# Kernel tuning notes

Measured on AMD Instinct MI355X. Metric: run time of the kernel, lower is better.

The kernel has to match this reference:

```python
import jax, jax.numpy as jnp
import numpy as np

B_SZ, L, D = 8, 8192, 256


def setup_inputs() -> dict:
    key = jax.random.key(0)
    kx, ka, kb, kc = jax.random.split(key, 4)
    x = jax.random.normal(kx, (B_SZ, L, D), dtype=jnp.float32)
    # Scale A so its spectral radius is < 1; otherwise the 8192-step linear
    # recurrence overflows. (Random Gaussian DxD with std s has norm ~ 2*s*sqrt(D).)
    A = jax.random.normal(ka, (D, D), dtype=jnp.float32) * (0.4 / np.sqrt(D))
    B = jax.random.normal(kb, (D, D), dtype=jnp.float32) * 0.05
    C = jax.random.normal(kc, (D, D), dtype=jnp.float32) * 0.05
    return {"x": x, "A": A, "B": B, "C": C}


def reference(x, A, B, C):
    # state_t = state_{t-1} @ A + x_t @ B.T ; out_t = state_t @ C.T
    # Dropout is identity in eval mode and omitted.
    b = x.shape[0]
    h = A.shape[0]
    init = jnp.zeros((b, h), dtype=x.dtype)
    Bt = B.T  # (input_dim, hidden_dim) -> math uses x @ B.T per source
    Ct = C.T

    def step(state, xt):  # xt: (b, d)
        state = state @ A + xt @ Bt
        return state, state @ Ct

    _, ys = jax.lax.scan(step, init, jnp.swapaxes(x, 0, 1))  # ys: (l, b, out)
    return jnp.swapaxes(ys, 0, 1)  # (b, l, out)
```

## Files before the change

### kernel.cpp

```cpp
#include <hip/hip_runtime.h>

#define BSZ 8
#define LSEQ 8192
#define DDIM 256
#define CHUNK 16
#define WARM 32
#define STEPS (CHUNK + WARM)
#define CPB 16

typedef float f32x4 __attribute__((ext_vector_type(4)));
typedef _Float16 h8 __attribute__((ext_vector_type(8)));
typedef _Float16 h4 __attribute__((ext_vector_type(4)));
typedef _Float16 h2 __attribute__((ext_vector_type(2)));


__global__ void k_cvt_mats(const float* __restrict__ A, const float* __restrict__ B,
                           const float* __restrict__ C, _Float16* __restrict__ AhT,
                           _Float16* __restrict__ Bh, _Float16* __restrict__ Ch,
                           float* __restrict__ Zp) {
  int r = blockIdx.x, c = threadIdx.x;
  AhT[c * 256 + r] = (_Float16)A[r * 256 + c];
  Bh[r * 256 + c] = (_Float16)B[r * 256 + c];
  Ch[r * 256 + c] = (_Float16)C[r * 256 + c];
  if (r == 0) Zp[c] = 0.f;
}

__global__ __launch_bounds__(256, 2) void k_gemm_u(const float* __restrict__ x,
                                                   const _Float16* __restrict__ Bh,
                                                   _Float16* __restrict__ U) {
  __shared__ __align__(16) _Float16 xh[128][264];
  const int tid = threadIdx.x, wv = tid >> 6, lane = tid & 63;
  const int l15 = lane & 15, q = lane >> 4;
  const size_t rowbase = (size_t)blockIdx.x * 128;
#pragma unroll
  for (int i = 0; i < 32; ++i) {
    const int f4 = i * 256 + tid;
    const int row = f4 >> 6, c4 = f4 & 63;
    float4 v = *(const float4*)(x + (rowbase + row) * 256 + c4 * 4);
    h4 h;
    h[0] = (_Float16)v.x; h[1] = (_Float16)v.y; h[2] = (_Float16)v.z; h[3] = (_Float16)v.w;
    *(h4*)&xh[row][c4 * 4] = h;
  }
  __syncthreads();
#pragma unroll 1
  for (int cbk = 0; cbk < 4; ++cbk) {
    h8 bf[4][8];
#pragma unroll
    for (int ct = 0; ct < 4; ++ct)
#pragma unroll
      for (int kb = 0; kb < 8; ++kb)
        bf[ct][kb] = *(const h8*)(Bh + (size_t)(cbk * 64 + ct * 16 + l15) * 256 + kb * 32 + q * 8);
#pragma unroll
    for (int rt = 0; rt < 2; ++rt) {
      const int rloc = wv * 32 + rt * 16;
      f32x4 acc[4] = {};
#pragma unroll
      for (int kb = 0; kb < 8; ++kb) {
        h8 af = *(const h8*)&xh[rloc + l15][kb * 32 + q * 8];
#pragma unroll
        for (int ct = 0; ct < 4; ++ct)
          acc[ct] = __builtin_amdgcn_mfma_f32_16x16x32_f16(af, bf[ct][kb], acc[ct], 0, 0, 0);
      }
      const size_t grow = rowbase + rloc + q * 4;
#pragma unroll
      for (int r = 0; r < 4; ++r) {
        h4 hv;
        hv[0] = (_Float16)acc[0][r]; hv[1] = (_Float16)acc[1][r];
        hv[2] = (_Float16)acc[2][r]; hv[3] = (_Float16)acc[3][r];
        *(h4*)(U + (grow + r) * 256 + cbk * 64 + l15 * 4) = hv;
      }
    }
  }
}

__global__ __launch_bounds__(512, 2) void k_scan(const _Float16* __restrict__ U,
                                                 const _Float16* __restrict__ AhT,
                                                 const _Float16* __restrict__ Ch,
                                                 const _Float16* __restrict__ Zp,
                                                 float* __restrict__ O) {
  __shared__ __align__(16) _Float16 st[2][CPB][264];
  const int tid = threadIdx.x, wv = tid >> 6, lane = tid & 63;
  const int l15 = lane & 15, q = lane >> 4;
  const int g64 = wv >> 1, hf = wv & 1;
  const int b = blockIdx.x >> 5;
  const int c0 = (blockIdx.x & 31) * CPB;
  const size_t bbase = (size_t)b * LSEQ;

  h8 bf[2][8], cf[2][8];
#pragma unroll
  for (int ctl = 0; ctl < 2; ++ctl)
#pragma unroll
    for (int kb = 0; kb < 8; ++kb) {
      const size_t mo = (size_t)(g64 * 64 + (2 * hf + ctl) * 16 + l15) * 256 + kb * 32 + q * 8;
      bf[ctl][kb] = *(const h8*)(AhT + mo);
      cf[ctl][kb] = *(const h8*)(Ch + mo);
    }

  for (int i = tid; i < CPB * 264; i += 512) ((_Float16*)st[0])[i] = (_Float16)0.f;

  auto uload = [&](int t, int r) -> h2 {
    const int lr = (c0 + q * 4 + r) * CHUNK + t;
    const _Float16* p = (lr < 0 || lr >= LSEQ)
                            ? (Zp + l15 * 4 + 2 * hf)
                            : (U + (bbase + (size_t)lr) * 256 + g64 * 64 + l15 * 4 + 2 * hf);
    return *(const h2*)p;
  };

  float* op[4];
#pragma unroll
  for (int r = 0; r < 4; ++r)
    op[r] = O + (bbase + (size_t)(c0 + q * 4 + r) * CHUNK) * 256 + g64 * 64 + 2 * hf * 16 + l15;

  h2 up0 = uload(-WARM, 0), up1 = uload(-WARM, 1), up2 = uload(-WARM, 2), up3 = uload(-WARM, 3);
  __syncthreads();

  int cb = 0;
#pragma unroll 1
  for (int g = 0; g <= STEPS; ++g) {
    const int t = g - WARM;
    h2 un0 = uload(t + 1, 0), un1 = uload(t + 1, 1), un2 = uload(t + 1, 2), un3 = uload(t + 1, 3);
    if (g < STEPS) {
      f32x4 acc[2];
#pragma unroll
      for (int ctl = 0; ctl < 2; ++ctl) {
        acc[ctl][0] = (float)up0[ctl]; acc[ctl][1] = (float)up1[ctl];
        acc[ctl][2] = (float)up2[ctl]; acc[ctl][3] = (float)up3[ctl];
      }
      if (t >= 1) {
        f32x4 acc2[2] = {};
#pragma unroll
        for (int kb = 0; kb < 8; ++kb) {
          h8 af = *(const h8*)&st[cb][l15][kb * 32 + q * 8];
#pragma unroll
          for (int ctl = 0; ctl < 2; ++ctl)
            acc[ctl] = __builtin_amdgcn_mfma_f32_16x16x32_f16(af, bf[ctl][kb], acc[ctl], 0, 0, 0);
#pragma unroll
          for (int ctl = 0; ctl < 2; ++ctl)
            acc2[ctl] = __builtin_amdgcn_mfma_f32_16x16x32_f16(af, cf[ctl][kb], acc2[ctl], 0, 0, 0);
        }
#pragma unroll
        for (int ctl = 0; ctl < 2; ++ctl)
#pragma unroll
          for (int r = 0; r < 4; ++r)
            st[cb ^ 1][q * 4 + r][g64 * 64 + (2 * hf + ctl) * 16 + l15] = (_Float16)acc[ctl][r];
#pragma unroll
        for (int r = 0; r < 4; ++r) {
          op[r][0] = acc2[0][r];
          op[r][16] = acc2[1][r];
          op[r] += 256;
        }
      } else {
#pragma unroll
        for (int kb = 0; kb < 8; ++kb) {
          h8 af = *(const h8*)&st[cb][l15][kb * 32 + q * 8];
#pragma unroll
          for (int ctl = 0; ctl < 2; ++ctl)
            acc[ctl] = __builtin_amdgcn_mfma_f32_16x16x32_f16(af, bf[ctl][kb], acc[ctl], 0, 0, 0);
        }
#pragma unroll
        for (int ctl = 0; ctl < 2; ++ctl)
#pragma unroll
          for (int r = 0; r < 4; ++r)
            st[cb ^ 1][q * 4 + r][g64 * 64 + (2 * hf + ctl) * 16 + l15] = (_Float16)acc[ctl][r];
      }
    } else {
      f32x4 acc2[2] = {};
#pragma unroll
      for (int kb = 0; kb < 8; ++kb) {
        h8 af = *(const h8*)&st[cb][l15][kb * 32 + q * 8];
#pragma unroll
        for (int ctl = 0; ctl < 2; ++ctl)
          acc2[ctl] = __builtin_amdgcn_mfma_f32_16x16x32_f16(af, cf[ctl][kb], acc2[ctl], 0, 0, 0);
      }
#pragma unroll
      for (int r = 0; r < 4; ++r) {
        op[r][0] = acc2[0][r];
        op[r][16] = acc2[1][r];
      }
    }
    asm volatile("s_waitcnt lgkmcnt(0)" ::: "memory");
    __builtin_amdgcn_s_barrier();
    asm volatile("" ::: "memory");
    up0 = un0; up1 = un1; up2 = un2; up3 = un3;
    cb ^= 1;
  }
}

extern "C" void kernel_launch(void* const* d_in, const int* in_sizes, int n_in,
                              void* d_out, int out_size, void* d_ws, size_t ws_size,
                              hipStream_t stream) {
  const float* x = (const float*)d_in[0];
  const float* A = (const float*)d_in[1];
  const float* B = (const float*)d_in[2];
  const float* C = (const float*)d_in[3];

  char* ws = (char*)d_ws;
  _Float16* U4 = (_Float16*)ws;
  _Float16* AhT = (_Float16*)(ws + 33554432);
  _Float16* Bh = (_Float16*)(ws + 33554432 + 131072);
  _Float16* Ch = (_Float16*)(ws + 33554432 + 262144);
  float* Zp = (float*)(ws + 33554432 + 393216);
  float* out = (float*)d_out;

  hipLaunchKernelGGL(k_cvt_mats, dim3(256), dim3(256), 0, stream, A, B, C, AhT, Bh, Ch, Zp);
  hipLaunchKernelGGL(k_gemm_u, dim3(512), dim3(256), 0, stream, x, Bh, U4);
  hipLaunchKernelGGL(k_scan, dim3(256), dim3(512), 0, stream, U4, AhT, Ch,
                     (const _Float16*)Zp, out);
}
```

Baseline: 184.2 us.

## Fold matrix conversion into projection GEMM and deepen scan input prefetch

Removes the separate conversion kernel. The first 256 GEMM blocks now convert A (transposed) and C to fp16, and B is read directly as fp32 and converted in registers inside the GEMM. The B fragments are loaded in two halves to cut register use, and the launch-bound occupancy hints are dropped. The scan kernel splits warmup and main loops, prefetches U two steps ahead, and replaces the out-of-range zero-pointer branch in the main loop with an index clamp. Together this saves a launch and some branch cost, but it adds redundant fp32 B loads per block and relies on the scan reading AhT/Ch written by an earlier kernel in the same stream.

After: 211.5 us. 14.8% more time.

```diff
diff --git a/kernel.cpp b/kernel.cpp
--- a/kernel.cpp
+++ b/kernel.cpp
@@ -14,23 +14,22 @@
 typedef _Float16 h2 __attribute__((ext_vector_type(2)));
 
 
-__global__ void k_cvt_mats(const float* __restrict__ A, const float* __restrict__ B,
-                           const float* __restrict__ C, _Float16* __restrict__ AhT,
-                           _Float16* __restrict__ Bh, _Float16* __restrict__ Ch,
-                           float* __restrict__ Zp) {
-  int r = blockIdx.x, c = threadIdx.x;
-  AhT[c * 256 + r] = (_Float16)A[r * 256 + c];
-  Bh[r * 256 + c] = (_Float16)B[r * 256 + c];
-  Ch[r * 256 + c] = (_Float16)C[r * 256 + c];
-  if (r == 0) Zp[c] = 0.f;
-}
-
-__global__ __launch_bounds__(256, 2) void k_gemm_u(const float* __restrict__ x,
-                                                   const _Float16* __restrict__ Bh,
-                                                   _Float16* __restrict__ U) {
+__global__ __launch_bounds__(256) void k_gemm_u(
+    const float* __restrict__ x, const float* __restrict__ A,
+    const float* __restrict__ B, const float* __restrict__ C,
+    _Float16* __restrict__ U, _Float16* __restrict__ AhT,
+    _Float16* __restrict__ Ch, _Float16* __restrict__ Zph) {
   __shared__ __align__(16) _Float16 xh[128][264];
   const int tid = threadIdx.x, wv = tid >> 6, lane = tid & 63;
   const int l15 = lane & 15, q = lane >> 4;
+
+  if (blockIdx.x < 256) {
+    const int r = blockIdx.x;
+    AhT[tid * 256 + r] = (_Float16)A[r * 256 + tid];
+    Ch[r * 256 + tid] = (_Float16)C[r * 256 + tid];
+    if (r == 0) { Zph[tid] = (_Float16)0.f; Zph[tid + 256] = (_Float16)0.f; }
+  }
+
   const size_t rowbase = (size_t)blockIdx.x * 128;
 #pragma unroll
   for (int i = 0; i < 32; ++i) {
@@ -42,42 +41,52 @@
     *(h4*)&xh[row][c4 * 4] = h;
   }
   __syncthreads();
+
 #pragma unroll 1
   for (int cbk = 0; cbk < 4; ++cbk) {
-    h8 bf[4][8];
-#pragma unroll
-    for (int ct = 0; ct < 4; ++ct)
-#pragma unroll
-      for (int kb = 0; kb < 8; ++kb)
-        bf[ct][kb] = *(const h8*)(Bh + (size_t)(cbk * 64 + ct * 16 + l15) * 256 + kb * 32 + q * 8);
-#pragma unroll
-    for (int rt = 0; rt < 2; ++rt) {
-      const int rloc = wv * 32 + rt * 16;
-      f32x4 acc[4] = {};
-#pragma unroll
-      for (int kb = 0; kb < 8; ++kb) {
-        h8 af = *(const h8*)&xh[rloc + l15][kb * 32 + q * 8];
-#pragma unroll
-        for (int ct = 0; ct < 4; ++ct)
-          acc[ct] = __builtin_amdgcn_mfma_f32_16x16x32_f16(af, bf[ct][kb], acc[ct], 0, 0, 0);
-      }
-      const size_t grow = rowbase + rloc + q * 4;
-#pragma unroll
-      for (int r = 0; r < 4; ++r) {
-        h4 hv;
-        hv[0] = (_Float16)acc[0][r]; hv[1] = (_Float16)acc[1][r];
-        hv[2] = (_Float16)acc[2][r]; hv[3] = (_Float16)acc[3][r];
-        *(h4*)(U + (grow + r) * 256 + cbk * 64 + l15 * 4) = hv;
+#pragma unroll 1
+    for (int ch = 0; ch < 2; ++ch) {
+      h8 bf[2][8];
+#pragma unroll
+      for (int ctl = 0; ctl < 2; ++ctl)
+#pragma unroll
+        for (int kb = 0; kb < 8; ++kb) {
+          const float* bp =
+              B + (size_t)(cbk * 64 + (2 * ch + ctl) * 16 + l15) * 256 + kb * 32 + q * 8;
+          float4 b0 = *(const float4*)bp, b1 = *(const float4*)(bp + 4);
+          h8 f;
+          f[0] = (_Float16)b0.x; f[1] = (_Float16)b0.y; f[2] = (_Float16)b0.z; f[3] = (_Float16)b0.w;
+          f[4] = (_Float16)b1.x; f[5] = (_Float16)b1.y; f[6] = (_Float16)b1.z; f[7] = (_Float16)b1.w;
+          bf[ctl][kb] = f;
+        }
+#pragma unroll
+      for (int rt = 0; rt < 2; ++rt) {
+        const int rloc = wv * 32 + rt * 16;
+        f32x4 acc[2] = {};
+#pragma unroll
+        for (int kb = 0; kb < 8; ++kb) {
+          h8 af = *(const h8*)&xh[rloc + l15][kb * 32 + q * 8];
+#pragma unroll
+          for (int ctl = 0; ctl < 2; ++ctl)
+            acc[ctl] = __builtin_amdgcn_mfma_f32_16x16x32_f16(af, bf[ctl][kb], acc[ctl], 0, 0, 0);
+        }
+        const size_t grow = rowbase + rloc + q * 4;
+#pragma unroll
+        for (int r = 0; r < 4; ++r) {
+          h2 hv;
+          hv[0] = (_Float16)acc[0][r]; hv[1] = (_Float16)acc[1][r];
+          *(h2*)(U + (grow + r) * 256 + cbk * 64 + l15 * 4 + 2 * ch) = hv;
+        }
       }
     }
   }
 }
 
-__global__ __launch_bounds__(512, 2) void k_scan(const _Float16* __restrict__ U,
-                                                 const _Float16* __restrict__ AhT,
-                                                 const _Float16* __restrict__ Ch,
-                                                 const _Float16* __restrict__ Zp,
-                                                 float* __restrict__ O) {
+__global__ __launch_bounds__(512) void k_scan(const _Float16* __restrict__ U,
+                                              const _Float16* __restrict__ AhT,
+                                              const _Float16* __restrict__ Ch,
+                                              const _Float16* __restrict__ Zph,
+                                              float* __restrict__ O) {
   __shared__ __align__(16) _Float16 st[2][CPB][264];
   const int tid = threadIdx.x, wv = tid >> 6, lane = tid & 63;
   const int l15 = lane & 15, q = lane >> 4;
@@ -98,27 +107,66 @@
 
   for (int i = tid; i < CPB * 264; i += 512) ((_Float16*)st[0])[i] = (_Float16)0.f;
 
-  auto uload = [&](int t, int r) -> h2 {
+  const int coff = g64 * 64 + l15 * 4 + 2 * hf;
+  auto uload_w = [&](int t, int r) -> h2 {
     const int lr = (c0 + q * 4 + r) * CHUNK + t;
-    const _Float16* p = (lr < 0 || lr >= LSEQ)
-                            ? (Zp + l15 * 4 + 2 * hf)
-                            : (U + (bbase + (size_t)lr) * 256 + g64 * 64 + l15 * 4 + 2 * hf);
+    const _Float16* p = (lr < 0) ? (Zph + l15 * 4 + 2 * hf)
+                                 : (U + (bbase + (size_t)lr) * 256 + coff);
     return *(const h2*)p;
   };
+  auto uload_m = [&](int t, int r) -> h2 {
+    int lr = (c0 + q * 4 + r) * CHUNK + t;
+    lr = lr > (LSEQ - 1) ? (LSEQ - 1) : lr;
+    return *(const h2*)(U + (bbase + (size_t)lr) * 256 + coff);
+  };
 
   float* op[4];
 #pragma unroll
   for (int r = 0; r < 4; ++r)
     op[r] = O + (bbase + (size_t)(c0 + q * 4 + r) * CHUNK) * 256 + g64 * 64 + 2 * hf * 16 + l15;
 
-  h2 up0 = uload(-WARM, 0), up1 = uload(-WARM, 1), up2 = uload(-WARM, 2), up3 = uload(-WARM, 3);
+  h2 up0 = uload_w(-WARM, 0), up1 = uload_w(-WARM, 1);
+  h2 up2 = uload_w(-WARM, 2), up3 = uload_w(-WARM, 3);
+  h2 un0 = uload_w(-WARM + 1, 0), un1 = uload_w(-WARM + 1, 1);
+  h2 un2 = uload_w(-WARM + 1, 2), un3 = uload_w(-WARM + 1, 3);
   __syncthreads();
 
   int cb = 0;
 #pragma unroll 1
-  for (int g = 0; g <= STEPS; ++g) {
+  for (int g = 0; g < WARM; ++g) {
     const int t = g - WARM;
-    h2 un0 = uload(t + 1, 0), un1 = uload(t + 1, 1), un2 = uload(t + 1, 2), un3 = uload(t + 1, 3);
+    h2 uf0 = uload_w(t + 2, 0), uf1 = uload_w(t + 2, 1);
+    h2 uf2 = uload_w(t + 2, 2), uf3 = uload_w(t + 2, 3);
+    f32x4 acc[2];
+#pragma unroll
+    for (int ctl = 0; ctl < 2; ++ctl) {
+      acc[ctl][0] = (float)up0[ctl]; acc[ctl][1] = (float)up1[ctl];
+      acc[ctl][2] = (float)up2[ctl]; acc[ctl][3] = (float)up3[ctl];
+    }
+#pragma unroll
+    for (int kb = 0; kb < 8; ++kb) {
+      h8 af = *(const h8*)&st[cb][l15][kb * 32 + q * 8];
+#pragma unroll
+      for (int ctl = 0; ctl < 2; ++ctl)
+        acc[ctl] = __builtin_amdgcn_mfma_f32_16x16x32_f16(af, bf[ctl][kb], acc[ctl], 0, 0, 0);
+    }
+#pragma unroll
+    for (int ctl = 0; ctl < 2; ++ctl)
+#pragma unroll
+      for (int r = 0; r < 4; ++r)
+        st[cb ^ 1][q * 4 + r][g64 * 64 + (2 * hf + ctl) * 16 + l15] = (_Float16)acc[ctl][r];
+    asm volatile("s_waitcnt lgkmcnt(0)" ::: "memory");
+    __builtin_amdgcn_s_barrier();
+    asm volatile("" ::: "memory");
+    up0 = un0; up1 = un1; up2 = un2; up3 = un3;
+    un0 = uf0; un1 = uf1; un2 = uf2; un3 = uf3;
+    cb ^= 1;
+  }
+#pragma unroll 1
+  for (int g = WARM; g <= STEPS; ++g) {
+    const int t = g - WARM;
+    h2 uf0 = uload_m(t + 2, 0), uf1 = uload_m(t + 2, 1);
+    h2 uf2 = uload_m(t + 2, 2), uf3 = uload_m(t + 2, 3);
     if (g < STEPS) {
       f32x4 acc[2];
 #pragma unroll
@@ -182,6 +230,7 @@
     __builtin_amdgcn_s_barrier();
     asm volatile("" ::: "memory");
     up0 = un0; up1 = un1; up2 = un2; up3 = un3;
+    un0 = uf0; un1 = uf1; un2 = uf2; un3 = uf3;
     cb ^= 1;
   }
 }
@@ -195,15 +244,13 @@
   const float* C = (const float*)d_in[3];
 
   char* ws = (char*)d_ws;
-  _Float16* U4 = (_Float16*)ws;
+  _Float16* U = (_Float16*)ws;
   _Float16* AhT = (_Float16*)(ws + 33554432);
-  _Float16* Bh = (_Float16*)(ws + 33554432 + 131072);
-  _Float16* Ch = (_Float16*)(ws + 33554432 + 262144);
-  float* Zp = (float*)(ws + 33554432 + 393216);
+  _Float16* Ch = (_Float16*)(ws + 33554432 + 131072);
+  _Float16* Zph = (_Float16*)(ws + 33554432 + 262144);
   float* out = (float*)d_out;
 
-  hipLaunchKernelGGL(k_cvt_mats, dim3(256), dim3(256), 0, stream, A, B, C, AhT, Bh, Ch, Zp);
-  hipLaunchKernelGGL(k_gemm_u, dim3(512), dim3(256), 0, stream, x, Bh, U4);
-  hipLaunchKernelGGL(k_scan, dim3(256), dim3(512), 0, stream, U4, AhT, Ch,
-                     (const _Float16*)Zp, out);
+  hipLaunchKernelGGL(k_gemm_u, dim3(512), dim3(256), 0, stream, x, A, B, C, U, AhT,
+                     Ch, Zph);
+  hipLaunchKernelGGL(k_scan, dim3(256), dim3(512), 0, stream, U, AhT, Ch, Zph, out);
 }
```

## Fuse matrix conversion into input GEMM and stage B through shared memory

Applied to the files above, without the earlier changes.

Removes the separate conversion kernel: the GEMM kernel now converts A and C to fp16 in its first 256 blocks and converts B on the fly into shared memory per column block instead of reading a pre-converted fp16 copy from global. The GEMM tile shrinks from 128 to 64 rows, doubling the grid to 1024 blocks, with B fragments read from LDS rather than held in registers. This saves one launch and a global round trip for B, at the cost of re-reading and re-converting fp32 B in every block and adding extra barriers. Reusing the first barrier to also cover the x staging keeps correctness.

New measurement: 178.0 us. -3.4%, faster.

```diff
diff --git a/kernel.cpp b/kernel.cpp
--- a/kernel.cpp
+++ b/kernel.cpp
@@ -14,26 +14,26 @@
 typedef _Float16 h2 __attribute__((ext_vector_type(2)));
 
 
-__global__ void k_cvt_mats(const float* __restrict__ A, const float* __restrict__ B,
-                           const float* __restrict__ C, _Float16* __restrict__ AhT,
-                           _Float16* __restrict__ Bh, _Float16* __restrict__ Ch,
-                           float* __restrict__ Zp) {
-  int r = blockIdx.x, c = threadIdx.x;
-  AhT[c * 256 + r] = (_Float16)A[r * 256 + c];
-  Bh[r * 256 + c] = (_Float16)B[r * 256 + c];
-  Ch[r * 256 + c] = (_Float16)C[r * 256 + c];
-  if (r == 0) Zp[c] = 0.f;
-}
-
-__global__ __launch_bounds__(256, 2) void k_gemm_u(const float* __restrict__ x,
-                                                   const _Float16* __restrict__ Bh,
-                                                   _Float16* __restrict__ U) {
-  __shared__ __align__(16) _Float16 xh[128][264];
+__global__ __launch_bounds__(256) void k_gemm_u(
+    const float* __restrict__ x, const float* __restrict__ A,
+    const float* __restrict__ B, const float* __restrict__ C,
+    _Float16* __restrict__ U, _Float16* __restrict__ AhT,
+    _Float16* __restrict__ Ch, _Float16* __restrict__ Zph) {
+  __shared__ __align__(16) _Float16 xh[64][264];
+  __shared__ __align__(16) _Float16 bs[64][264];
   const int tid = threadIdx.x, wv = tid >> 6, lane = tid & 63;
   const int l15 = lane & 15, q = lane >> 4;
-  const size_t rowbase = (size_t)blockIdx.x * 128;
-#pragma unroll
-  for (int i = 0; i < 32; ++i) {
+
+  if (blockIdx.x < 256) {
+    const int r = blockIdx.x;
+    AhT[tid * 256 + r] = (_Float16)A[r * 256 + tid];
+    Ch[r * 256 + tid] = (_Float16)C[r * 256 + tid];
+    if (r == 0) { Zph[tid] = (_Float16)0.f; Zph[tid + 256] = (_Float16)0.f; }
+  }
+
+  const size_t rowbase = (size_t)blockIdx.x * 64;
+#pragma unroll 4
+  for (int i = 0; i < 16; ++i) {
     const int f4 = i * 256 + tid;
     const int row = f4 >> 6, c4 = f4 & 63;
     float4 v = *(const float4*)(x + (rowbase + row) * 256 + c4 * 4);
@@ -41,34 +41,38 @@
     h[0] = (_Float16)v.x; h[1] = (_Float16)v.y; h[2] = (_Float16)v.z; h[3] = (_Float16)v.w;
     *(h4*)&xh[row][c4 * 4] = h;
   }
-  __syncthreads();
+
 #pragma unroll 1
   for (int cbk = 0; cbk < 4; ++cbk) {
-    h8 bf[4][8];
-#pragma unroll
-    for (int ct = 0; ct < 4; ++ct)
-#pragma unroll
-      for (int kb = 0; kb < 8; ++kb)
-        bf[ct][kb] = *(const h8*)(Bh + (size_t)(cbk * 64 + ct * 16 + l15) * 256 + kb * 32 + q * 8);
-#pragma unroll
-    for (int rt = 0; rt < 2; ++rt) {
-      const int rloc = wv * 32 + rt * 16;
-      f32x4 acc[4] = {};
-#pragma unroll
-      for (int kb = 0; kb < 8; ++kb) {
-        h8 af = *(const h8*)&xh[rloc + l15][kb * 32 + q * 8];
-#pragma unroll
-        for (int ct = 0; ct < 4; ++ct)
-          acc[ct] = __builtin_amdgcn_mfma_f32_16x16x32_f16(af, bf[ct][kb], acc[ct], 0, 0, 0);
-      }
-      const size_t grow = rowbase + rloc + q * 4;
-#pragma unroll
-      for (int r = 0; r < 4; ++r) {
-        h4 hv;
-        hv[0] = (_Float16)acc[0][r]; hv[1] = (_Float16)acc[1][r];
-        hv[2] = (_Float16)acc[2][r]; hv[3] = (_Float16)acc[3][r];
-        *(h4*)(U + (grow + r) * 256 + cbk * 64 + l15 * 4) = hv;
-      }
+    __syncthreads();
+#pragma unroll 4
+    for (int i = 0; i < 16; ++i) {
+      const int f4 = i * 256 + tid;
+      const int row = f4 >> 6, c4 = f4 & 63;
+      float4 v = *(const float4*)(B + (size_t)(cbk * 64 + row) * 256 + c4 * 4);
+      h4 h;
+      h[0] = (_Float16)v.x; h[1] = (_Float16)v.y; h[2] = (_Float16)v.z; h[3] = (_Float16)v.w;
+      *(h4*)&bs[row][c4 * 4] = h;
+    }
+    __syncthreads();
+
+    f32x4 acc[4] = {};
+#pragma unroll
+    for (int kb = 0; kb < 8; ++kb) {
+      h8 af = *(const h8*)&xh[wv * 16 + l15][kb * 32 + q * 8];
+#pragma unroll
+      for (int ct = 0; ct < 4; ++ct) {
+        h8 bf = *(const h8*)&bs[ct * 16 + l15][kb * 32 + q * 8];
+        acc[ct] = __builtin_amdgcn_mfma_f32_16x16x32_f16(af, bf, acc[ct], 0, 0, 0);
+      }
+    }
+    const size_t grow = rowbase + wv * 16 + q * 4;
+#pragma unroll
+    for (int r = 0; r < 4; ++r) {
+      h4 hv;
+      hv[0] = (_Float16)acc[0][r]; hv[1] = (_Float16)acc[1][r];
+      hv[2] = (_Float16)acc[2][r]; hv[3] = (_Float16)acc[3][r];
+      *(h4*)(U + (grow + r) * 256 + cbk * 64 + l15 * 4) = hv;
     }
   }
 }
@@ -195,15 +199,13 @@
   const float* C = (const float*)d_in[3];
 
   char* ws = (char*)d_ws;
-  _Float16* U4 = (_Float16*)ws;
+  _Float16* U = (_Float16*)ws;
   _Float16* AhT = (_Float16*)(ws + 33554432);
-  _Float16* Bh = (_Float16*)(ws + 33554432 + 131072);
-  _Float16* Ch = (_Float16*)(ws + 33554432 + 262144);
-  float* Zp = (float*)(ws + 33554432 + 393216);
+  _Float16* Ch = (_Float16*)(ws + 33554432 + 131072);
+  _Float16* Zph = (_Float16*)(ws + 33554432 + 262144);
   float* out = (float*)d_out;
 
-  hipLaunchKernelGGL(k_cvt_mats, dim3(256), dim3(256), 0, stream, A, B, C, AhT, Bh, Ch, Zp);
-  hipLaunchKernelGGL(k_gemm_u, dim3(512), dim3(256), 0, stream, x, Bh, U4);
-  hipLaunchKernelGGL(k_scan, dim3(256), dim3(512), 0, stream, U4, AhT, Ch,
-                     (const _Float16*)Zp, out);
+  hipLaunchKernelGGL(k_gemm_u, dim3(1024), dim3(256), 0, stream, x, A, B, C, U, AhT,
+                     Ch, Zph);
+  hipLaunchKernelGGL(k_scan, dim3(256), dim3(512), 0, stream, U, AhT, Ch, Zph, out);
 }
```
